# Kernel optimization log

Measured on AMD Instinct MI355X. Metric: run time of the kernel, lower is better.

Reference implementation:

```python
import jax, jax.numpy as jnp
import numpy as np
from jax import lax

H = 50  # hidden size fixed by the module


def setup_inputs() -> dict:
    key = jax.random.key(0)
    ks = jax.random.split(key, 7)
    B, T, I = 512, 1000, 64
    s = 0.1
    return {
        "x": jax.random.normal(ks[0], (B, T, I), dtype=jnp.float32),
        "W_ih": jax.random.normal(ks[1], (4 * H, I), dtype=jnp.float32) * s,
        "W_hh": jax.random.normal(ks[2], (4 * H, H), dtype=jnp.float32) * s,
        "b_ih": jax.random.normal(ks[3], (4 * H,), dtype=jnp.float32) * s,
        "b_hh": jax.random.normal(ks[4], (4 * H,), dtype=jnp.float32) * s,
        "W_out": jax.random.normal(ks[5], (2, H), dtype=jnp.float32) * s,
        "b_out": jax.random.normal(ks[6], (2,), dtype=jnp.float32) * s,
    }


def _lstm_last_h(x, W_ih, W_hh, b_ih, b_hh):
    # x: [B, T, I]. Precompute input contribution to all gates: [B, T, 4H]
    xg = jnp.einsum("bti,gi->btg", x, W_ih) + b_ih + b_hh
    B = x.shape[0]
    h0 = jnp.zeros((B, H), dtype=x.dtype)
    c0 = jnp.zeros((B, H), dtype=x.dtype)

    def step(carry, xt):
        h, c = carry
        gates = xt + h @ W_hh.T  # [B, 4H]
        i, f, g, o = jnp.split(gates, 4, axis=-1)  # torch gate order i,f,g,o
        i = jax.nn.sigmoid(i)
        f = jax.nn.sigmoid(f)
        g = jnp.tanh(g)
        o = jax.nn.sigmoid(o)
        c = f * c + i * g
        h = o * jnp.tanh(c)
        return (h, c), None

    (h_last, _), _ = lax.scan(step, (h0, c0), jnp.swapaxes(xg, 0, 1))
    return h_last  # [B, H]


def reference(x, W_ih, W_hh, b_ih, b_hh, W_out, b_out):
    h = _lstm_last_h(x, W_ih, W_hh, b_ih, b_hh)
    return h @ W_out.T + b_out  # [B, 2]
```

## Files before the change

### kernel.cpp

```cpp
#include <hip/hip_runtime.h>
#include <math.h>


#define HSZ 50
#define ISZ 64
#define TSZ 1000

typedef float f32x2 __attribute__((ext_vector_type(2)));

__device__ __forceinline__ float dpp_xor1(float v) {
    return __int_as_float(__builtin_amdgcn_update_dpp(
        0, __float_as_int(v), 0xB1, 0xF, 0xF, true));
}
__device__ __forceinline__ float dpp_xor2(float v) {
    return __int_as_float(__builtin_amdgcn_update_dpp(
        0, __float_as_int(v), 0x4E, 0xF, 0xF, true));
}

#define LSTM_STEP(t, OFF, XR)                                                  \
  {                                                                            \
    if (tid < 256) {                                                           \
      if (tid < 200) {                                                         \
        float acc0 = xgbuf[(OFF) & 3][k];                                      \
        const f32x2* h2 = (const f32x2*)(&hbuf[(OFF) & 1][0]);                 \
        f32x2 accA; accA.x = acc0; accA.y = 0.0f;                              \
        f32x2 accB; accB.x = 0.0f; accB.y = 0.0f;                              \
        _Pragma("unroll")                                                      \
        for (int j = 0; j < 12; ++j) {                                         \
          accA += h2[2 * j]     * wreg[2 * j];                                 \
          accB += h2[2 * j + 1] * wreg[2 * j + 1];                             \
        }                                                                      \
        accA += h2[24] * wreg[24];                            \
        float acc = (accA.x + accB.x) + (accA.y + accB.y);                     \
        float arg = isg ? (acc + acc) : acc;                                   \
        float e = __expf(-arg);                                                \
        float sg = __fdividef(1.0f, 1.0f + e);                                 \
        float a = isg ? (sg + sg - 1.0f) : sg;                                 \
        float bb = dpp_xor1(a);                                                \
        float cv = dpp_xor2(a);                                                \
        float dv = dpp_xor2(bb);                                               \
        float xlo = b0 ? bb : a,  xhi = b0 ? a : bb;                           \
        float ylo = b0 ? dv : cv, yhi = b0 ? cv : dv;                          \
        float ig = b1 ? ylo : xlo, fg = b1 ? yhi : xhi;                        \
        float gg = b1 ? xlo : ylo, og = b1 ? xhi : yhi;                        \
        c_reg = fg * c_reg + ig * gg;                                          \
        float ep = __expf(c_reg + c_reg);                                      \
        float th = 1.0f - __fdividef(2.0f, 1.0f + ep);                         \
        if ((tid & 3) == 0) hbuf[((OFF) + 1) & 1][u] = og * th;                \
      }                                                                        \
    } else if (P < 200) {                                                      \
      if ((t) + (OFF) + 2 < TSZ) {                                             \
        const f32x2* x2 = (const f32x2*)(&xbuf[((OFF) + 2) & 3][0]);           \
        f32x2 accA; accA.x = bias; accA.y = 0.0f;                              \
        f32x2 accB; accB.x = 0.0f; accB.y = 0.0f;                              \
        _Pragma("unroll")                                                      \
        for (int i = 0; i < 16; ++i) {                                         \
          accA += x2[2 * i]     * wreg[2 * i];                                 \
          accB += x2[2 * i + 1] * wreg[2 * i + 1];                             \
        }                                                                      \
        xgbuf[((OFF) + 2) & 3][P] = (accA.x + accB.x) + (accA.y + accB.y);     \
      }                                                                        \
    } else if (ll >= 0) {                                                      \
      if ((t) + (OFF) + 3 < TSZ)                                               \
        *(f32x2*)(&xbuf[((OFF) + 3) & 3][2 * ll]) = XR;                        \
      if ((t) + (OFF) + 5 < TSZ)                                               \
        XR = *(const f32x2*)(xb + (size_t)((t) + (OFF) + 5) * ISZ + 2 * ll);   \
    }                                                                          \
    asm volatile("s_waitcnt lgkmcnt(0)" ::: "memory");                         \
    __builtin_amdgcn_s_barrier();                                              \
    __builtin_amdgcn_sched_barrier(0);                                         \
  }

__global__ __launch_bounds__(512, 4) void lstm_fused(
    const float* __restrict__ x,
    const float* __restrict__ W_ih,
    const float* __restrict__ W_hh,
    const float* __restrict__ b_ih,
    const float* __restrict__ b_hh,
    const float* __restrict__ W_out,
    const float* __restrict__ b_out,
    float* __restrict__ out)
{
    const int b   = blockIdx.x;
    const int tid = threadIdx.x;

    __shared__ __align__(16) float xbuf[4][ISZ];
    __shared__ __align__(16) float xgbuf[4][200];
    __shared__ __align__(16) float hbuf[2][56];

    const int g = tid & 3;
    const int u = tid >> 2;
    const int k = g * HSZ + u;
    const bool isg = (g == 2);
    const bool b0  = (g & 1) != 0;
    const bool b1  = (g & 2) != 0;

    const int P  = tid - 256;
    const int ll = P - 224;

    f32x2 wreg[32];
    float bias  = 0.0f;
    float c_reg = 0.0f;
    f32x2 xr0; xr0.x = 0.0f; xr0.y = 0.0f;
    f32x2 xr1; xr1.x = 0.0f; xr1.y = 0.0f;

    const float* xb = x + (size_t)b * (TSZ * ISZ);

    if (tid < 200) {
        const float* wh = W_hh + k * HSZ;
        #pragma unroll
        for (int j = 0; j < 25; ++j) wreg[j] = *(const f32x2*)(wh + 2 * j);
    } else if (tid >= 256 && P < 200) {
        const float* wi = W_ih + P * ISZ;
        #pragma unroll
        for (int i = 0; i < 32; ++i) wreg[i] = *(const f32x2*)(wi + 2 * i);
        bias = b_ih[P] + b_hh[P];
    } else if (ll >= 0) {
        #pragma unroll
        for (int n = 0; n < 3; ++n) {
            f32x2 v = *(const f32x2*)(xb + n * ISZ + 2 * ll);
            *(f32x2*)(&xbuf[n][2 * ll]) = v;
        }
        xr0 = *(const f32x2*)(xb + 3 * ISZ + 2 * ll);
        xr1 = *(const f32x2*)(xb + 4 * ISZ + 2 * ll);
    }
    if (tid < HSZ) { hbuf[0][tid] = 0.0f; hbuf[1][tid] = 0.0f; }
    __syncthreads();

    if (tid >= 256 && P < 200) {
        #pragma unroll
        for (int n = 0; n < 2; ++n) {
            const f32x2* x2 = (const f32x2*)(&xbuf[n][0]);
            f32x2 accA; accA.x = bias; accA.y = 0.0f;
            f32x2 accB; accB.x = 0.0f; accB.y = 0.0f;
            #pragma unroll
            for (int i = 0; i < 16; ++i) {
                accA += x2[2 * i]     * wreg[2 * i];
                accB += x2[2 * i + 1] * wreg[2 * i + 1];
            }
            xgbuf[n][P] = (accA.x + accB.x) + (accA.y + accB.y);
        }
    }
    __syncthreads();

    for (int t = 0; t < TSZ; t += 4) {
        LSTM_STEP(t, 0, xr0)
        LSTM_STEP(t, 1, xr1)
        LSTM_STEP(t, 2, xr0)
        LSTM_STEP(t, 3, xr1)
    }

    if (tid < 2) {
        float acc = b_out[tid];
        const float* wo = W_out + tid * HSZ;
        #pragma unroll
        for (int j = 0; j < HSZ; ++j) acc += hbuf[0][j] * wo[j];
        out[b * 2 + tid] = acc;
    }
}

extern "C" void kernel_launch(void* const* d_in, const int* in_sizes, int n_in,
                              void* d_out, int out_size, void* d_ws, size_t ws_size,
                              hipStream_t stream) {
    const float* x     = (const float*)d_in[0];
    const float* W_ih  = (const float*)d_in[1];
    const float* W_hh  = (const float*)d_in[2];
    const float* b_ih  = (const float*)d_in[3];
    const float* b_hh  = (const float*)d_in[4];
    const float* W_out = (const float*)d_in[5];
    const float* b_out = (const float*)d_in[6];
    float* out = (float*)d_out;

    const int B = in_sizes[0] / (TSZ * ISZ);
    hipLaunchKernelGGL(lstm_fused, dim3(B), dim3(512), 0, stream,
                       x, W_ih, W_hh, b_ih, b_hh, W_out, b_out, out);
}
```

Baseline: 788.5 us.

## Process two batch rows per block and fuse input projection into recurrent threads

Each block now handles two sequences, one per 256-thread half. The same thread computes both the recurrent matvec and the next-step input projection, so the xgbuf shared buffer is gone and the projected input stays in registers. Gate gathering is simplified with a DPP row-reverse plus FMA-based sigmoid/tanh using rcp, and launch bounds are relaxed to allow more registers. The trade-off is a longer serial instruction stream per thread and half as many blocks, in exchange for less LDS traffic and fewer idle waves.

```diff
diff --git a/kernel.cpp b/kernel.cpp
--- a/kernel.cpp
+++ b/kernel.cpp
@@ -16,62 +16,68 @@
     return __int_as_float(__builtin_amdgcn_update_dpp(
         0, __float_as_int(v), 0x4E, 0xF, 0xF, true));
 }
+__device__ __forceinline__ float dpp_rev(float v) {
+    return __int_as_float(__builtin_amdgcn_update_dpp(
+        0, __float_as_int(v), 0x1B, 0xF, 0xF, true));
+}
 
-#define LSTM_STEP(t, OFF, XR)                                                  \
+#define LSTM_STEP(t, OFF, XR, XG)                                              \
   {                                                                            \
-    if (tid < 256) {                                                           \
-      if (tid < 200) {                                                         \
-        float acc0 = xgbuf[(OFF) & 3][k];                                      \
-        const f32x2* h2 = (const f32x2*)(&hbuf[(OFF) & 1][0]);                 \
-        f32x2 accA; accA.x = acc0; accA.y = 0.0f;                              \
-        f32x2 accB; accB.x = 0.0f; accB.y = 0.0f;                              \
-        _Pragma("unroll")                                                      \
-        for (int j = 0; j < 12; ++j) {                                         \
-          accA += h2[2 * j]     * wreg[2 * j];                                 \
-          accB += h2[2 * j + 1] * wreg[2 * j + 1];                             \
-        }                                                                      \
-        accA += h2[24] * wreg[24];                            \
-        float acc = (accA.x + accB.x) + (accA.y + accB.y);                     \
-        float arg = isg ? (acc + acc) : acc;                                   \
-        float e = __expf(-arg);                                                \
-        float sg = __fdividef(1.0f, 1.0f + e);                                 \
-        float a = isg ? (sg + sg - 1.0f) : sg;                                 \
-        float bb = dpp_xor1(a);                                                \
-        float cv = dpp_xor2(a);                                                \
-        float dv = dpp_xor2(bb);                                               \
-        float xlo = b0 ? bb : a,  xhi = b0 ? a : bb;                           \
-        float ylo = b0 ? dv : cv, yhi = b0 ? cv : dv;                          \
-        float ig = b1 ? ylo : xlo, fg = b1 ? yhi : xhi;                        \
-        float gg = b1 ? xlo : ylo, og = b1 ? xhi : yhi;                        \
-        c_reg = fg * c_reg + ig * gg;                                          \
-        float ep = __expf(c_reg + c_reg);                                      \
-        float th = 1.0f - __fdividef(2.0f, 1.0f + ep);                         \
-        if ((tid & 3) == 0) hbuf[((OFF) + 1) & 1][u] = og * th;                \
+    if (rtid < 200) {                                                          \
+                                      \
+      f32x2 accA; accA.x = XG; accA.y = 0.0f;                                  \
+      f32x2 accB; accB.x = 0.0f; accB.y = 0.0f;                                \
+      const float4* h4 = (const float4*)(&hbuf[row][(OFF) & 1][0]);            \
+      _Pragma("unroll")                                                        \
+      for (int j = 0; j < 12; ++j) {                                           \
+        float4 v = h4[j];                                                      \
+        f32x2 lo; lo.x = v.x; lo.y = v.y;                                      \
+        f32x2 hi; hi.x = v.z; hi.y = v.w;                                      \
+        accA += lo * whh[2 * j];                                               \
+        accB += hi * whh[2 * j + 1];                                           \
       }                                                                        \
-    } else if (P < 200) {                                                      \
+      { f32x2 tl = *(const f32x2*)(&hbuf[row][(OFF) & 1][48]);                 \
+        accA += tl * whh[24]; }                                                \
+      float acc = (accA.x + accB.x) + (accA.y + accB.y);                       \
+      float e  = __expf(-(acc * gmul));                                        \
+      float sg = __builtin_amdgcn_rcpf(1.0f + e);                              \
+      float a  = __builtin_fmaf(sg, gma, gmb);            \
+      float fg = dpp_xor1(a);                 \
+      float gg = dpp_xor2(a);                 \
+      float og = dpp_rev(a);                  \
+      c_reg = __builtin_fmaf(fg, c_reg, a * gg);      \
+      float ep = __expf(2.0f * c_reg);                                         \
+      float rr = __builtin_amdgcn_rcpf(1.0f + ep);                             \
+      float hv = __builtin_fmaf(-2.0f * og, rr, og);         \
+      if ((rtid & 3) == 0) hbuf[row][((OFF) + 1) & 1][u] = hv;                 \
+            \
       if ((t) + (OFF) + 2 < TSZ) {                                             \
-        const f32x2* x2 = (const f32x2*)(&xbuf[((OFF) + 2) & 3][0]);           \
-        f32x2 accA; accA.x = bias; accA.y = 0.0f;                              \
-        f32x2 accB; accB.x = 0.0f; accB.y = 0.0f;                              \
+        f32x2 pA; pA.x = bias; pA.y = 0.0f;                                    \
+        f32x2 pB; pB.x = 0.0f; pB.y = 0.0f;                                    \
+        const float4* x4 = (const float4*)(&xbuf[row][((OFF) + 2) & 3][0]);    \
         _Pragma("unroll")                                                      \
         for (int i = 0; i < 16; ++i) {                                         \
-          accA += x2[2 * i]     * wreg[2 * i];                                 \
-          accB += x2[2 * i + 1] * wreg[2 * i + 1];                             \
+          float4 v = x4[i];                                                    \
+          f32x2 lo; lo.x = v.x; lo.y = v.y;                                    \
+          f32x2 hi; hi.x = v.z; hi.y = v.w;                                    \
+          pA += lo * wih[2 * i];                                               \
+          pB += hi * wih[2 * i + 1];                                           \
         }                                                                      \
-        xgbuf[((OFF) + 2) & 3][P] = (accA.x + accB.x) + (accA.y + accB.y);     \
+        XG = (pA.x + pB.x) + (pA.y + pB.y);                                    \
       }                                                                        \
-    } else if (ll >= 0) {                                                      \
+    } else if (rtid >= 224) {                                                  \
       if ((t) + (OFF) + 3 < TSZ)                                               \
-        *(f32x2*)(&xbuf[((OFF) + 3) & 3][2 * ll]) = XR;                        \
+        *(f32x2*)(&xbuf[row][((OFF) + 3) & 3][2 * ll]) = XR;                   \
       if ((t) + (OFF) + 5 < TSZ)                                               \
-        XR = *(const f32x2*)(xb + (size_t)((t) + (OFF) + 5) * ISZ + 2 * ll);   \
+        XR = *(const f32x2*)(xrow + (size_t)((t) + (OFF) + 5) * ISZ + 2 * ll); \
     }                                                                          \
+                     \
     asm volatile("s_waitcnt lgkmcnt(0)" ::: "memory");                         \
     __builtin_amdgcn_s_barrier();                                              \
     __builtin_amdgcn_sched_barrier(0);                                         \
   }
 
-__global__ __launch_bounds__(512, 4) void lstm_fused(
+__global__ __launch_bounds__(512, 2) void lstm_fused(
     const float* __restrict__ x,
     const float* __restrict__ W_ih,
     const float* __restrict__ W_hh,
@@ -81,81 +87,85 @@
     const float* __restrict__ b_out,
     float* __restrict__ out)
 {
-    const int b   = blockIdx.x;
-    const int tid = threadIdx.x;
+    const int bb   = blockIdx.x;
+    const int tid  = threadIdx.x;
+    const int row  = tid >> 8;
+    const int rtid = tid & 255;
 
-    __shared__ __align__(16) float xbuf[4][ISZ];
-    __shared__ __align__(16) float xgbuf[4][200];
-    __shared__ __align__(16) float hbuf[2][56];
+    __shared__ __align__(16) float xbuf[2][4][ISZ];
+    __shared__ __align__(16) float hbuf[2][2][56];
 
-    const int g = tid & 3;
-    const int u = tid >> 2;
+    const int g = rtid & 3;
+    const int u = rtid >> 2;
     const int k = g * HSZ + u;
-    const bool isg = (g == 2);
-    const bool b0  = (g & 1) != 0;
-    const bool b1  = (g & 2) != 0;
+    const float gmul = (g == 2) ? 2.0f : 1.0f;
+    const float gma  = (g == 2) ? 2.0f : 1.0f;
+    const float gmb  = (g == 2) ? -1.0f : 0.0f;
 
-    const int P  = tid - 256;
-    const int ll = P - 224;
+    const int ll = rtid - 224;
 
-    f32x2 wreg[32];
+    const float* xrow = x + (size_t)(2 * bb + row) * (TSZ * ISZ);
+
+    f32x2 whh[25];
+    f32x2 wih[32];
     float bias  = 0.0f;
     float c_reg = 0.0f;
+    float xgA = 0.0f, xgB = 0.0f;
     f32x2 xr0; xr0.x = 0.0f; xr0.y = 0.0f;
     f32x2 xr1; xr1.x = 0.0f; xr1.y = 0.0f;
 
-    const float* xb = x + (size_t)b * (TSZ * ISZ);
-
-    if (tid < 200) {
+    if (rtid < 200) {
         const float* wh = W_hh + k * HSZ;
         #pragma unroll
-        for (int j = 0; j < 25; ++j) wreg[j] = *(const f32x2*)(wh + 2 * j);
-    } else if (tid >= 256 && P < 200) {
-        const float* wi = W_ih + P * ISZ;
+        for (int j = 0; j < 25; ++j) whh[j] = *(const f32x2*)(wh + 2 * j);
+        const float* wi = W_ih + k * ISZ;
         #pragma unroll
-        for (int i = 0; i < 32; ++i) wreg[i] = *(const f32x2*)(wi + 2 * i);
-        bias = b_ih[P] + b_hh[P];
+        for (int i = 0; i < 32; ++i) wih[i] = *(const f32x2*)(wi + 2 * i);
+        bias = b_ih[k] + b_hh[k];
     } else if (ll >= 0) {
         #pragma unroll
         for (int n = 0; n < 3; ++n) {
-            f32x2 v = *(const f32x2*)(xb + n * ISZ + 2 * ll);
-            *(f32x2*)(&xbuf[n][2 * ll]) = v;
+            f32x2 v = *(const f32x2*)(xrow + n * ISZ + 2 * ll);
+            *(f32x2*)(&xbuf[row][n][2 * ll]) = v;
         }
-        xr0 = *(const f32x2*)(xb + 3 * ISZ + 2 * ll);
-        xr1 = *(const f32x2*)(xb + 4 * ISZ + 2 * ll);
+        xr0 = *(const f32x2*)(xrow + 3 * ISZ + 2 * ll);
+        xr1 = *(const f32x2*)(xrow + 4 * ISZ + 2 * ll);
     }
-    if (tid < HSZ) { hbuf[0][tid] = 0.0f; hbuf[1][tid] = 0.0f; }
+    if (rtid < 56) { hbuf[row][0][rtid] = 0.0f; hbuf[row][1][rtid] = 0.0f; }
     __syncthreads();
 
-    if (tid >= 256 && P < 200) {
+    if (rtid < 200) {
         #pragma unroll
         for (int n = 0; n < 2; ++n) {
-            const f32x2* x2 = (const f32x2*)(&xbuf[n][0]);
-            f32x2 accA; accA.x = bias; accA.y = 0.0f;
-            f32x2 accB; accB.x = 0.0f; accB.y = 0.0f;
+            f32x2 pA; pA.x = bias; pA.y = 0.0f;
+            f32x2 pB; pB.x = 0.0f; pB.y = 0.0f;
+            const float4* x4 = (const float4*)(&xbuf[row][n][0]);
             #pragma unroll
             for (int i = 0; i < 16; ++i) {
-                accA += x2[2 * i]     * wreg[2 * i];
-                accB += x2[2 * i + 1] * wreg[2 * i + 1];
+                float4 v = x4[i];
+                f32x2 lo; lo.x = v.x; lo.y = v.y;
+                f32x2 hi; hi.x = v.z; hi.y = v.w;
+                pA += lo * wih[2 * i];
+                pB += hi * wih[2 * i + 1];
             }
-            xgbuf[n][P] = (accA.x + accB.x) + (accA.y + accB.y);
+            float r = (pA.x + pB.x) + (pA.y + pB.y);
+            if (n == 0) xgA = r; else xgB = r;
         }
     }
-    __syncthreads();
 
     for (int t = 0; t < TSZ; t += 4) {
-        LSTM_STEP(t, 0, xr0)
-        LSTM_STEP(t, 1, xr1)
-        LSTM_STEP(t, 2, xr0)
-        LSTM_STEP(t, 3, xr1)
+        LSTM_STEP(t, 0, xr0, xgA)
+        LSTM_STEP(t, 1, xr1, xgB)
+        LSTM_STEP(t, 2, xr0, xgA)
+        LSTM_STEP(t, 3, xr1, xgB)
     }
 
-    if (tid < 2) {
-        float acc = b_out[tid];
-        const float* wo = W_out + tid * HSZ;
+    if (rtid < 2) {
+        float acc = b_out[rtid];
+        const float* wo = W_out + rtid * HSZ;
         #pragma unroll
-        for (int j = 0; j < HSZ; ++j) acc += hbuf[0][j] * wo[j];
-        out[b * 2 + tid] = acc;
+        for (int j = 0; j < HSZ; ++j) acc += hbuf[row][0][j] * wo[j];
+        out[(2 * bb + row) * 2 + rtid] = acc;
     }
 }
 
@@ -172,6 +182,6 @@
     float* out = (float*)d_out;
 
     const int B = in_sizes[0] / (TSZ * ISZ);
-    hipLaunchKernelGGL(lstm_fused, dim3(B), dim3(512), 0, stream,
+    hipLaunchKernelGGL(lstm_fused, dim3(B / 2), dim3(512), 0, stream,
                        x, W_ih, W_hh, b_ih, b_hh, W_out, b_out, out);
 }
```

After: 771.2 us. 2.2% less time.
